# Optimization experiments

Measured on AMD Instinct MI355X. Metric: run time of the kernel, lower is better.

The kernel has to match this reference:

```python
import jax, jax.numpy as jnp
import numpy as np
from jax import lax

BIG = 1e8  # sentinel 'infinity'; safe in fp32 since max (i-j)^2 ~ 512^2


def _dt1d(f, axis):
    """Exact 1-D squared-distance transform along `axis`:
    d[i] = min_j (i-j)^2 + f[j]. Scanned over j (min-plus), fully vectorized
    over all other dims."""
    f = jnp.moveaxis(f, axis, -1)
    shp = f.shape
    n = shp[-1]
    fr = f.reshape(-1, n)  # [R, n]
    idx = jnp.arange(n, dtype=f.dtype)

    def step(d, xs):
        fj, j = xs  # fj: [R], j: scalar position
        cand = fj[:, None] + (idx - j) ** 2  # [R, n]
        return jnp.minimum(d, cand), None

    d0 = jnp.full_like(fr, BIG)
    d, _ = lax.scan(step, d0, (fr.T, idx))
    return jnp.moveaxis(d.reshape(shp), -1, axis)


def _edt(mask):
    """Exact Euclidean distance transform: distance from every element to the
    nearest True element of `mask` (0 where mask is True). Matches
    scipy.ndimage.distance_transform_edt(~mask applied as in the torch module)
    via the exact separable squared-distance decomposition, over ALL dims
    (including batch/channel, as the original code does)."""
    f = jnp.where(mask, 0.0, BIG).astype(jnp.float32)
    for ax in range(f.ndim):
        f = _dt1d(f, ax)
    return jnp.sqrt(f)


def setup_inputs() -> dict:
    key = jax.random.key(0)
    k1, k2 = jax.random.split(key)
    shape = (8, 1, 512, 512)
    x = jax.random.normal(k1, shape, dtype=jnp.float32)
    # sparse binary label mask (~1/64 foreground) for non-trivial distances
    y = (jax.random.randint(k2, shape, 0, 64) == 0).astype(jnp.int32)
    return {"x": x, "y": y}


def reference(x, y):
    # original: dist = EDT(logical_not(y)) = distance to nearest nonzero of y
    d = _edt(y != 0)
    return (jax.nn.sigmoid(x) * d).mean()
```

## Files before the change

kernel.cpp:

```cpp
#include <hip/hip_runtime.h>
#include <math.h>

#define BIGV  1.0e8f
#define PLANE (512 * 512)
#define NTOT  (8 * PLANE)
#define PROWS 640
#define PSTRIDE (PROWS * 512)

__global__ __launch_bounds__(512) void dt_axis3(const int* __restrict__ y,
                                                float* __restrict__ g1p) {
    int blk = blockIdx.x;
    if (blk >= 4096) {
        int idx = (blk - 4096) * 512 + threadIdx.x;
        int plane = idx >> 16;
        int rem   = idx & 65535;
        int r     = rem >> 9;
        int c     = rem & 511;
        int row   = (r < 64) ? r : (r + 512);
        g1p[plane * PSTRIDE + row * 512 + c] = BIGV;
        return;
    }
    __shared__ unsigned long long words[8];
    int i = threadIdx.x;
    int e = blk * 512 + i;
    unsigned long long bal = __ballot(y[e] != 0);
    int wid  = i >> 6;
    int lane = i & 63;
    if (lane == 0) words[wid] = bal;
    __syncthreads();

    int k = wid, b = lane;
    int dr = 1 << 30;
    {
        unsigned long long m0 = words[k] & (~0ull << b);
        if (m0) {
            dr = (__ffsll((long long)m0) - 1) - b;
        } else {
            #pragma unroll
            for (int k2 = 0; k2 < 8; ++k2) {
                if (k2 > k && dr == (1 << 30) && words[k2]) {
                    dr = (k2 << 6) + (__ffsll((long long)words[k2]) - 1) - i;
                }
            }
        }
    }
    int dl = 1 << 30;
    {
        unsigned long long m0 = words[k] & (~0ull >> (63 - b));
        if (m0) {
            dl = b - (63 - __clzll((long long)m0));
        } else {
            #pragma unroll
            for (int k2 = 7; k2 >= 0; --k2) {
                if (k2 < k && dl == (1 << 30) && words[k2]) {
                    dl = i - ((k2 << 6) + 63 - __clzll((long long)words[k2]));
                }
            }
        }
    }
    int d = min(dl, dr);
    float h2 = (d > 511) ? BIGV : (float)(d * d);
    int bb = blk >> 9, i2 = blk & 511;
    g1p[bb * PSTRIDE + (64 + i2) * 512 + i] = h2;
}

__global__ __launch_bounds__(256) void dt_axis2(const float* __restrict__ g1p,
                                                float* __restrict__ D2) {
    int e = blockIdx.x * 256 + threadIdx.x;
    int b   = e >> 18;
    int rem = e & (PLANE - 1);
    int i2  = rem >> 9;
    int i3  = rem & 511;
    const float* base = g1p + b * PSTRIDE + (64 + i2) * 512 + i3;

    float m  = *base;
    float au = base[-512];
    float ad = base[+512];
    const float* up = base - 512;
    const float* dn = base + 512;
    float fr2 = 1.0f, dstep = 3.0f;
    int r = 1;
    for (; r < 64; ++r) {
        if (fr2 >= m) break;
        float cand = fminf(au, ad) + fr2;
        au = up[-512]; ad = dn[+512];
        up -= 512; dn += 512;
        m = fminf(m, cand);
        fr2 += dstep; dstep += 2.0f;
    }
    if (r == 64) {
        for (; r < 512; ++r) {
            float f2 = (float)(r * r);
            if (f2 >= m) break;
            int upr = i2 - r, dnr = i2 + r;
            if (upr < 0 && dnr >= 512) break;
            if (upr >= 0)  m = fminf(m, g1p[b * PSTRIDE + (64 + upr) * 512 + i3] + f2);
            if (dnr < 512) m = fminf(m, g1p[b * PSTRIDE + (64 + dnr) * 512 + i3] + f2);
        }
    }
    D2[e] = m;
}

__device__ inline double wave_reduce_d(double v) {
    #pragma unroll
    for (int off = 32; off > 0; off >>= 1) v += __shfl_down(v, off, 64);
    return v;
}

__global__ __launch_bounds__(256) void axis0_epilogue(const float* __restrict__ D2,
                                                      const float* __restrict__ x,
                                                      double* __restrict__ partials) {
    int s = blockIdx.x * 256 + threadIdx.x;
    float v[8];
    #pragma unroll
    for (int b = 0; b < 8; ++b) v[b] = D2[b * PLANE + s];

    double acc = 0.0;
    #pragma unroll
    for (int b = 0; b < 8; ++b) {
        float m = BIGV;
        #pragma unroll
        for (int bp = 0; bp < 8; ++bp) {
            float db = (float)((b - bp) * (b - bp));
            m = fminf(m, v[bp] + db);
        }
        float xv  = x[b * PLANE + s];
        float sig = 1.0f / (1.0f + expf(-xv));
        acc += (double)(sig * sqrtf(m));
    }

    __shared__ double lds[4];
    double w = wave_reduce_d(acc);
    int lane = threadIdx.x & 63;
    int wid  = threadIdx.x >> 6;
    if (lane == 0) lds[wid] = w;
    __syncthreads();
    if (wid == 0) {
        double t = (lane < 4) ? lds[lane] : 0.0;
        #pragma unroll
        for (int off = 2; off > 0; off >>= 1) t += __shfl_down(t, off, 64);
        if (lane == 0) partials[blockIdx.x] = t;
    }
}

__global__ __launch_bounds__(256) void finalize(const double* __restrict__ partials,
                                                float* __restrict__ out) {
    double a = 0.0;
    for (int i = threadIdx.x; i < 1024; i += 256) a += partials[i];
    __shared__ double lds[4];
    double w = wave_reduce_d(a);
    int lane = threadIdx.x & 63;
    int wid  = threadIdx.x >> 6;
    if (lane == 0) lds[wid] = w;
    __syncthreads();
    if (threadIdx.x == 0) {
        double total = lds[0] + lds[1] + lds[2] + lds[3];
        out[0] = (float)(total / (double)NTOT);
    }
}

extern "C" void kernel_launch(void* const* d_in, const int* in_sizes, int n_in,
                              void* d_out, int out_size, void* d_ws, size_t ws_size,
                              hipStream_t stream) {
    const float* x = (const float*)d_in[0];
    const int*   y = (const int*)d_in[1];
    float* out = (float*)d_out;

    float*  g1p      = (float*)d_ws;
    float*  D2       = g1p + 8 * PSTRIDE;
    double* partials = (double*)(D2 + NTOT);

    dt_axis3<<<5120, 512, 0, stream>>>(y, g1p);
    dt_axis2<<<NTOT / 256, 256, 0, stream>>>(g1p, D2);
    axis0_epilogue<<<PLANE / 256, 256, 0, stream>>>(D2, x, partials);
    finalize<<<1, 256, 0, stream>>>(partials, out);
}
```

Measured before the change: 96.80 us.

## Fuse column DT into batch-axis epilogue and store row distances as uint16

Row-pass distances are now stored as 16-bit integers (capped at a sentinel of 1023) instead of squared fp32 values, halving the intermediate's footprint. The column-direction transform is fused into the batch-axis epilogue kernel, so each thread computes all eight batch columns in registers and the D2 buffer plus one kernel launch are removed. The cost is that the fused kernel launches only 1024 blocks with eight sequential, data-dependent column scans per thread, which lowers parallelism and occupancy compared with the separate per-element launch.

Result: slower. 105.9 us (+9.4%).

```diff
diff --git a/kernel.cpp b/kernel.cpp
--- a/kernel.cpp
+++ b/kernel.cpp
@@ -6,9 +6,10 @@
 #define NTOT  (8 * PLANE)
 #define PROWS 640
 #define PSTRIDE (PROWS * 512)
+#define HSENT 1023
 
 __global__ __launch_bounds__(512) void dt_axis3(const int* __restrict__ y,
-                                                float* __restrict__ g1p) {
+                                                unsigned short* __restrict__ g1u) {
     int blk = blockIdx.x;
     if (blk >= 4096) {
         int idx = (blk - 4096) * 512 + threadIdx.x;
@@ -17,7 +18,7 @@
         int r     = rem >> 9;
         int c     = rem & 511;
         int row   = (r < 64) ? r : (r + 512);
-        g1p[plane * PSTRIDE + row * 512 + c] = BIGV;
+        g1u[plane * PSTRIDE + row * 512 + c] = HSENT;
         return;
     }
     __shared__ unsigned long long words[8];
@@ -59,46 +60,9 @@
         }
     }
     int d = min(dl, dr);
-    float h2 = (d > 511) ? BIGV : (float)(d * d);
+    int h = min(d, HSENT);
     int bb = blk >> 9, i2 = blk & 511;
-    g1p[bb * PSTRIDE + (64 + i2) * 512 + i] = h2;
-}
-
-__global__ __launch_bounds__(256) void dt_axis2(const float* __restrict__ g1p,
-                                                float* __restrict__ D2) {
-    int e = blockIdx.x * 256 + threadIdx.x;
-    int b   = e >> 18;
-    int rem = e & (PLANE - 1);
-    int i2  = rem >> 9;
-    int i3  = rem & 511;
-    const float* base = g1p + b * PSTRIDE + (64 + i2) * 512 + i3;
-
-    float m  = *base;
-    float au = base[-512];
-    float ad = base[+512];
-    const float* up = base - 512;
-    const float* dn = base + 512;
-    float fr2 = 1.0f, dstep = 3.0f;
-    int r = 1;
-    for (; r < 64; ++r) {
-        if (fr2 >= m) break;
-        float cand = fminf(au, ad) + fr2;
-        au = up[-512]; ad = dn[+512];
-        up -= 512; dn += 512;
-        m = fminf(m, cand);
-        fr2 += dstep; dstep += 2.0f;
-    }
-    if (r == 64) {
-        for (; r < 512; ++r) {
-            float f2 = (float)(r * r);
-            if (f2 >= m) break;
-            int upr = i2 - r, dnr = i2 + r;
-            if (upr < 0 && dnr >= 512) break;
-            if (upr >= 0)  m = fminf(m, g1p[b * PSTRIDE + (64 + upr) * 512 + i3] + f2);
-            if (dnr < 512) m = fminf(m, g1p[b * PSTRIDE + (64 + dnr) * 512 + i3] + f2);
-        }
-    }
-    D2[e] = m;
+    g1u[bb * PSTRIDE + (64 + i2) * 512 + i] = (unsigned short)h;
 }
 
 __device__ inline double wave_reduce_d(double v) {
@@ -107,13 +71,53 @@
     return v;
 }
 
-__global__ __launch_bounds__(256) void axis0_epilogue(const float* __restrict__ D2,
-                                                      const float* __restrict__ x,
-                                                      double* __restrict__ partials) {
-    int s = blockIdx.x * 256 + threadIdx.x;
+__global__ __launch_bounds__(256) void dt2_axis0_epilogue(
+        const unsigned short* __restrict__ g1u,
+        const float* __restrict__ x,
+        double* __restrict__ partials) {
+    int s  = blockIdx.x * 256 + threadIdx.x;
+    int i2 = s >> 9;
+    int i3 = s & 511;
+
     float v[8];
     #pragma unroll
-    for (int b = 0; b < 8; ++b) v[b] = D2[b * PLANE + s];
+    for (int bb = 0; bb < 8; ++bb) {
+        const unsigned short* base = g1u + bb * PSTRIDE + (64 + i2) * 512 + i3;
+        int h0  = base[0];
+        float m = (float)(h0 * h0);
+        int au = base[-512];
+        int ad = base[+512];
+        const unsigned short* up = base - 512;
+        const unsigned short* dn = base + 512;
+        float fr2 = 1.0f, dstep = 3.0f;
+        int r = 1;
+        for (; r < 64; ++r) {
+            if (fr2 >= m) break;
+            int hm = min(au, ad);
+            float cand = (float)(hm * hm) + fr2;
+            au = up[-512]; ad = dn[+512];
+            up -= 512; dn += 512;
+            m = fminf(m, cand);
+            fr2 += dstep; dstep += 2.0f;
+        }
+        if (r == 64) {
+            for (; r < 512; ++r) {
+                float f2 = (float)(r * r);
+                if (f2 >= m) break;
+                int upr = i2 - r, dnr = i2 + r;
+                if (upr < 0 && dnr >= 512) break;
+                if (upr >= 0) {
+                    int hh = g1u[bb * PSTRIDE + (64 + upr) * 512 + i3];
+                    m = fminf(m, (float)(hh * hh) + f2);
+                }
+                if (dnr < 512) {
+                    int hh = g1u[bb * PSTRIDE + (64 + dnr) * 512 + i3];
+                    m = fminf(m, (float)(hh * hh) + f2);
+                }
+            }
+        }
+        v[bb] = m;
+    }
 
     double acc = 0.0;
     #pragma unroll
@@ -166,12 +170,10 @@
     const int*   y = (const int*)d_in[1];
     float* out = (float*)d_out;
 
-    float*  g1p      = (float*)d_ws;
-    float*  D2       = g1p + 8 * PSTRIDE;
-    double* partials = (double*)(D2 + NTOT);
+    unsigned short* g1u = (unsigned short*)d_ws;
+    double* partials = (double*)((char*)d_ws + (size_t)8 * PSTRIDE * sizeof(unsigned short));
 
-    dt_axis3<<<5120, 512, 0, stream>>>(y, g1p);
-    dt_axis2<<<NTOT / 256, 256, 0, stream>>>(g1p, D2);
-    axis0_epilogue<<<PLANE / 256, 256, 0, stream>>>(D2, x, partials);
+    dt_axis3<<<5120, 512, 0, stream>>>(y, g1u);
+    dt2_axis0_epilogue<<<PLANE / 256, 256, 0, stream>>>(g1u, x, partials);
     finalize<<<1, 256, 0, stream>>>(partials, out);
 }
```
